# Kernel optimization log

Measured on AMD Instinct MI355X. Metric: run time of the kernel, lower is better.

The kernel has to match this reference:

```python
import jax, jax.numpy as jnp
import numpy as np

B, D, N, OUT, H = 32768, 256, 4, 512, 4
DH = D // H


def _layer_norm(x, g, b, eps=1e-5):
    mu = jnp.mean(x, axis=-1, keepdims=True)
    var = jnp.mean(jnp.square(x - mu), axis=-1, keepdims=True)
    return (x - mu) * jax.lax.rsqrt(var + eps) * g + b


def setup_inputs() -> dict:
    key = jax.random.key(0)
    ks = jax.random.split(key, 32)
    s = lambda i, shape, scale=0.02: (jax.random.normal(ks[i], shape, jnp.float32) * scale)
    inp = {
        'w0': jax.random.normal(ks[0], (B, D), jnp.float32),
        'w1': jax.random.normal(ks[1], (B, D), jnp.float32),
        'w2': jax.random.normal(ks[2], (B, D), jnp.float32),
        'w3': jax.random.normal(ks[3], (B, D), jnp.float32),
        'regime': jax.random.uniform(ks[4], (B, 4), jnp.float32),
        'tf_weights': jnp.array([0.5, 1.0, 1.5, 2.0], jnp.float32),
        'in_proj_w': s(5, (3 * D, D)),
        'in_proj_b': s(6, (3 * D,)),
        'out_proj_w': s(7, (D, D)),
        'out_proj_b': s(8, (D,)),
        'ln1_g': jnp.ones((D,), jnp.float32),
        'ln1_b': jnp.zeros((D,), jnp.float32),
        'sg_w': s(9, (D, 4)),
        'sg_b': s(10, (D,)),
        'sb_w': s(11, (D, 4)),
        'sb_b': s(12, (D,)),
        'f1_w': s(13, (2 * OUT, D * N)),
        'f1_b': s(14, (2 * OUT,)),
        'f2_w': s(15, (OUT, 2 * OUT)),
        'f2_b': s(16, (OUT,)),
        'ln2_g': jnp.ones((OUT,), jnp.float32),
        'ln2_b': jnp.zeros((OUT,), jnp.float32),
        'a1_w': s(17, (128, D * N)),
        'a1_b': s(18, (128,)),
        'a2_w': s(19, (1, 128)),
        'a2_b': s(20, (1,)),
    }
    return inp


def _forward(w0, w1, w2, w3, regime, tf_weights, in_proj_w, in_proj_b,
             out_proj_w, out_proj_b, ln1_g, ln1_b, sg_w, sg_b, sb_w, sb_b,
             f1_w, f1_b, f2_w, f2_b, ln2_g, ln2_b, a1_w, a1_b, a2_w, a2_b):
    weights = jax.nn.softmax(tf_weights)  # [N]
    wav = jnp.stack([w0, w1, w2, w3], axis=1)  # [B, N, D]
    weighted = wav * weights[None, :, None]    # [B, N, D]
    query = weighted[:, 0, :]                  # [B, D]

    # MultiheadAttention: q_len=1, kv_len=N, H heads
    wq, wk, wv = in_proj_w[:D], in_proj_w[D:2 * D], in_proj_w[2 * D:]
    bq, bk, bv = in_proj_b[:D], in_proj_b[D:2 * D], in_proj_b[2 * D:]
    q = (query @ wq.T + bq).reshape(B, H, DH)              # [B, H, Dh]
    k = (weighted @ wk.T + bk).reshape(B, N, H, DH)        # [B, N, H, Dh]
    v = (weighted @ wv.T + bv).reshape(B, N, H, DH)
    scores = jnp.einsum('bhd,bnhd->bhn', q, k) / jnp.sqrt(jnp.float32(DH))
    attn = jax.nn.softmax(scores, axis=-1)                 # [B, H, N]
    ctx = jnp.einsum('bhn,bnhd->bhd', attn, v).reshape(B, D)
    attn_out = ctx @ out_proj_w.T + out_proj_b             # [B, D]

    entry = _layer_norm(query + attn_out, ln1_g, ln1_b)    # [B, D]
    gamma = regime @ sg_w.T + sg_b
    beta = regime @ sb_w.T + sb_b
    entry = entry * (1.0 + gamma) + beta                   # FiLM

    cat = jnp.concatenate([entry, weighted[:, 1, :], weighted[:, 2, :], weighted[:, 3, :]], axis=-1)  # [B, D*N]
    h = jax.nn.gelu(cat @ f1_w.T + f1_b, approximate=False)
    fused = _layer_norm(h @ f2_w.T + f2_b, ln2_g, ln2_b)   # [B, OUT]

    a = jax.nn.gelu(cat @ a1_w.T + a1_b, approximate=False)
    alignment = jax.nn.sigmoid(a @ a2_w.T + a2_b)          # [B, 1]
    return fused, alignment


def reference(w0, w1, w2, w3, regime, tf_weights, in_proj_w, in_proj_b,
              out_proj_w, out_proj_b, ln1_g, ln1_b, sg_w, sg_b, sb_w, sb_b,
              f1_w, f1_b, f2_w, f2_b, ln2_g, ln2_b, a1_w, a1_b, a2_w, a2_b):
    return _forward(w0, w1, w2, w3, regime, tf_weights, in_proj_w, in_proj_b,
                    out_proj_w, out_proj_b, ln1_g, ln1_b, sg_w, sg_b, sb_w, sb_b,
                    f1_w, f1_b, f2_w, f2_b, ln2_g, ln2_b, a1_w, a1_b, a2_w, a2_b)
```

## Files before the change

kernel.cpp:

```cpp
#include <hip/hip_runtime.h>
#include <math.h>

#define NB 32768

typedef unsigned short u16;
typedef __attribute__((ext_vector_type(4))) float f32x4;
typedef __attribute__((ext_vector_type(8))) short bf16x8;

__device__ __forceinline__ float bf2f(u16 u){ return __uint_as_float(((unsigned int)u)<<16); }
__device__ __forceinline__ u16 f2bf(float f){
    unsigned int x = __float_as_uint(f);
    x += 0x7fffu + ((x>>16)&1u);
    return (u16)(x>>16);
}
__device__ __forceinline__ float gelu_f(float x){
    float z = fabsf(x) * 0.70710678118654752f;
    float t = __builtin_amdgcn_rcpf(1.0f + 0.3275911f*z);
    float p = t*(0.254829592f + t*(-0.284496736f + t*(1.421413741f + t*(-1.453152027f + t*1.061405429f))));
    float e = __expf(-z*z);
    float erf_abs = 1.0f - p*e;
    float erfv = copysignf(erf_abs, x);
    return 0.5f*x*(1.0f + erfv);
}

__device__ __forceinline__ void gload16(const void* g, void* l){
    __builtin_amdgcn_global_load_lds(
        (const __attribute__((address_space(1))) unsigned int*)g,
        (__attribute__((address_space(3))) unsigned int*)l, 16, 0, 0);
}

__global__ __launch_bounds__(256) void prep_kernel(
    const float* __restrict__ w0, const float* __restrict__ w1,
    const float* __restrict__ w2, const float* __restrict__ w3,
    const float* __restrict__ tfw, u16* __restrict__ wcat)
{
    float t0=tfw[0], t1=tfw[1], t2=tfw[2], t3=tfw[3];
    float m = fmaxf(fmaxf(t0,t1), fmaxf(t2,t3));
    float e0=expf(t0-m), e1=expf(t1-m), e2=expf(t2-m), e3=expf(t3-m);
    float inv = 1.0f/(e0+e1+e2+e3);
    float s0=e0*inv, s1=e1*inv, s2=e2*inv, s3=e3*inv;

    int idx = blockIdx.x*256 + threadIdx.x;
    int b  = idx >> 6;
    int d4 = (idx & 63) << 2;
    size_t src = (size_t)b*256 + d4;
    float4 a0 = *reinterpret_cast<const float4*>(w0 + src);
    float4 a1 = *reinterpret_cast<const float4*>(w1 + src);
    float4 a2 = *reinterpret_cast<const float4*>(w2 + src);
    float4 a3 = *reinterpret_cast<const float4*>(w3 + src);
    size_t dst = (size_t)b*1024 + d4;
    ushort4 o;
    o.x=f2bf(a0.x*s0); o.y=f2bf(a0.y*s0); o.z=f2bf(a0.z*s0); o.w=f2bf(a0.w*s0);
    *reinterpret_cast<ushort4*>(wcat + dst) = o;
    o.x=f2bf(a1.x*s1); o.y=f2bf(a1.y*s1); o.z=f2bf(a1.z*s1); o.w=f2bf(a1.w*s1);
    *reinterpret_cast<ushort4*>(wcat + dst + 256) = o;
    o.x=f2bf(a2.x*s2); o.y=f2bf(a2.y*s2); o.z=f2bf(a2.z*s2); o.w=f2bf(a2.w*s2);
    *reinterpret_cast<ushort4*>(wcat + dst + 512) = o;
    o.x=f2bf(a3.x*s3); o.y=f2bf(a3.y*s3); o.z=f2bf(a3.z*s3); o.w=f2bf(a3.w*s3);
    *reinterpret_cast<ushort4*>(wcat + dst + 768) = o;
}

__global__ __launch_bounds__(256) void conv1_kernel(const float* __restrict__ s, u16* __restrict__ d){
    int i = blockIdx.x*256 + threadIdx.x;
    float4 v = reinterpret_cast<const float4*>(s)[i];
    ushort4 o; o.x=f2bf(v.x); o.y=f2bf(v.y); o.z=f2bf(v.z); o.w=f2bf(v.w);
    reinterpret_cast<ushort4*>(d)[i] = o;
}

__global__ __launch_bounds__(256) void conv2_kernel(
    const float* __restrict__ s0, u16* __restrict__ d0,
    const float* __restrict__ s1, u16* __restrict__ d1,
    const float* __restrict__ s2, u16* __restrict__ d2,
    const float* __restrict__ s3, u16* __restrict__ d3)
{
    int i = blockIdx.x*256 + threadIdx.x;
    const float* s; u16* d; int off;
    if      (i < 16384) { s=s0; d=d0; off=i; }
    else if (i < 278528){ s=s1; d=d1; off=i-16384; }
    else if (i < 409600){ s=s2; d=d2; off=i-278528; }
    else                { s=s3; d=d3; off=i-409600; }
    float4 v = reinterpret_cast<const float4*>(s)[off];
    ushort4 o; o.x=f2bf(v.x); o.y=f2bf(v.y); o.z=f2bf(v.z); o.w=f2bf(v.w);
    reinterpret_cast<ushort4*>(d)[off] = o;
}

template<int ACT>
__global__ __launch_bounds__(256) void mgemm_kernel(
    const u16* __restrict__ A, int lda,
    const u16* __restrict__ W, int ldw,
    const float* __restrict__ bias,
    u16* __restrict__ C, int ldc, int K)
{
    __shared__ __align__(16) u16 sA[4096];
    __shared__ __align__(16) u16 sB[4096];

    const int tid  = threadIdx.x;
    const int lane = tid & 63;
    const int wid  = tid >> 6;
    const int wr   = wid >> 1, wc = wid & 1;
    const int row0 = blockIdx.x << 7, col0 = blockIdx.y << 7;

    const int e0 = tid << 3,          r0s = e0 >> 5, c0s = e0 & 31;
    const int e1 = (256 + tid) << 3,  r1s = e1 >> 5, c1s = e1 & 31;
    const u16* gA0 = A + (size_t)(row0 + r0s)*lda + c0s;
    const u16* gA1 = A + (size_t)(row0 + r1s)*lda + c1s;
    const u16* gB0 = W + (size_t)(col0 + r0s)*ldw + c0s;
    const u16* gB1 = W + (size_t)(col0 + r1s)*ldw + c1s;
    u16* lA0 = sA + (wid << 9);
    u16* lA1 = sA + 2048 + (wid << 9);
    u16* lB0 = sB + (wid << 9);
    u16* lB1 = sB + 2048 + (wid << 9);

    const int la  = lane & 15;
    const int lk  = (lane >> 4) << 3;
    const int hi4 = (lane >> 4) << 2;
    const u16* rA = sA + (((wr << 6) + la) << 5) + lk;
    const u16* rB = sB + (((wc << 6) + la) << 5) + lk;

    f32x4 acc[4][4];
    {
        f32x4 binit[4];
        #pragma unroll
        for (int n=0;n<4;n++){
            float4 b4 = *reinterpret_cast<const float4*>(bias + col0 + (wc<<6) + (n<<4) + hi4);
            binit[n] = (f32x4){b4.x, b4.y, b4.z, b4.w};
        }
        #pragma unroll
        for (int m=0;m<4;m++)
            #pragma unroll
            for (int n=0;n<4;n++) acc[m][n] = binit[n];
    }

    for (int k0 = 0; k0 < K; k0 += 32){
        gload16(gA0 + k0, lA0);
        gload16(gA1 + k0, lA1);
        gload16(gB0 + k0, lB0);
        gload16(gB1 + k0, lB1);
        __syncthreads();
        bf16x8 af[4], bf[4];
        #pragma unroll
        for (int m=0;m<4;m++) af[m] = *reinterpret_cast<const bf16x8*>(rA + (m << 9));
        #pragma unroll
        for (int n=0;n<4;n++) bf[n] = *reinterpret_cast<const bf16x8*>(rB + (n << 9));
        #pragma unroll
        for (int m=0;m<4;m++)
            #pragma unroll
            for (int n=0;n<4;n++)
                acc[m][n] = __builtin_amdgcn_mfma_f32_16x16x32_bf16(bf[n], af[m], acc[m][n], 0, 0, 0);
        __syncthreads();
    }

    #pragma unroll
    for (int m=0;m<4;m++){
        const int grow = row0 + (wr << 6) + (m << 4) + la;
        u16* crow = C + (size_t)grow*ldc + col0 + (wc << 6) + hi4;
        #pragma unroll
        for (int n=0;n<4;n++){
            f32x4 v = acc[m][n];
            float x0=v[0], x1=v[1], x2=v[2], x3=v[3];
            if (ACT == 1){ x0=gelu_f(x0); x1=gelu_f(x1); x2=gelu_f(x2); x3=gelu_f(x3); }
            ushort4 o; o.x=f2bf(x0); o.y=f2bf(x1); o.z=f2bf(x2); o.w=f2bf(x3);
            *reinterpret_cast<ushort4*>(crow + (n << 4)) = o;
        }
    }
}

template<int ACT>
__global__ __launch_bounds__(512) void gemm256p_kernel(
    const u16* __restrict__ A, int lda,
    const u16* __restrict__ W, int ldw,
    const float* __restrict__ bias,
    u16* __restrict__ C, int ldc, int K)
{
    __shared__ __align__(16) u16 sT[65536];

    const int tid  = threadIdx.x;
    const int lane = tid & 63;
    const int wid  = tid >> 6;
    const int wr   = wid >> 2;
    const int wc   = wid & 3;
    const int row0 = blockIdx.x << 8, col0 = blockIdx.y << 8;

    const int la = lane & 15;
    const int hi = lane >> 4;

    f32x4 acc[8][4];
    {
        f32x4 binit[4];
        #pragma unroll
        for (int n=0;n<4;n++){
            float4 b4 = *reinterpret_cast<const float4*>(bias + col0 + (wc<<6) + (n<<4) + (hi<<2));
            binit[n] = (f32x4){b4.x, b4.y, b4.z, b4.w};
        }
        #pragma unroll
        for (int m=0;m<8;m++)
            #pragma unroll
            for (int n=0;n<4;n++) acc[m][n] = binit[n];
    }

    const int rs = (wid << 4) + (lane >> 3);
    const int cs = ((lane & 7) ^ ((lane >> 3) & 7)) << 3;
    const u16* gA0 = A + (size_t)(row0 + rs)*lda + cs;
    const u16* gA1 = gA0 + (size_t)128*lda;
    const u16* gB0 = W + (size_t)(col0 + rs)*ldw + cs;
    const u16* gB1 = gB0 + (size_t)128*ldw;
    const int ldsw = (wid << 4) * 64;

    const int cph0 = (hi ^ (la & 7)) << 3;
    const u16* rAbase = sT + ((wr << 7) + la)*64;
    const u16* rBbase = sT + 16384 + ((wc << 6) + la)*64;

    const int NT = K >> 6;

    gload16(gB0, sT + 16384 + ldsw);          gload16(gB0 + 8*(size_t)ldw, sT + 16384 + ldsw + 512);
    gload16(gB1, sT + 16384 + 8192 + ldsw);   gload16(gB1 + 8*(size_t)ldw, sT + 16384 + 8192 + ldsw + 512);
    gload16(gA0, sT + ldsw);                  gload16(gA0 + 8*(size_t)lda, sT + ldsw + 512);
    gload16(gA1, sT + 8192 + ldsw);           gload16(gA1 + 8*(size_t)lda, sT + 8192 + ldsw + 512);

    for (int t = 0; t < NT; ++t){
        const int b  = (t & 1) << 15;
        const int bn = b ^ 32768;
        const int stg = (t + 1 < NT);
        const int kb = (t + 1) << 6;

#define STAGE_HALF(GP, LD, DOFF) \
        { gload16(GP + kb, sT + bn + (DOFF) + ldsw); \
          gload16(GP + kb + 8*(size_t)(LD), sT + bn + (DOFF) + ldsw + 512); }

#define PHASE(P) { \
        if ((P)==0){ \
            if (stg) { STAGE_HALF(gB0, ldw, 16384) } \
            if (stg) { asm volatile("s_waitcnt vmcnt(2)" ::: "memory"); } \
            else     { asm volatile("s_waitcnt vmcnt(0)" ::: "memory"); } \
        } \
        if ((P)==1 && stg) { STAGE_HALF(gB1, ldw, 16384 + 8192) } \
        if ((P)==2 && stg) { STAGE_HALF(gA0, lda, 0) } \
        if ((P)==3 && stg) { STAGE_HALF(gA1, lda, 8192) } \
        asm volatile("" ::: "memory"); \
        __builtin_amdgcn_s_barrier(); \
        __builtin_amdgcn_sched_barrier(0); \
        asm volatile("" ::: "memory"); \
        { \
            const int co = cph0 ^ (((P)>>1) << 5); \
            const u16* rA = rAbase + b + (((P)&1) << 12) + co; \
            const u16* rB = rBbase + b + co; \
            bf16x8 af0 = *reinterpret_cast<const bf16x8*>(rA); \
            bf16x8 af1 = *reinterpret_cast<const bf16x8*>(rA + 1024); \
            bf16x8 af2 = *reinterpret_cast<const bf16x8*>(rA + 2048); \
            bf16x8 af3 = *reinterpret_cast<const bf16x8*>(rA + 3072); \
            bf16x8 bf0 = *reinterpret_cast<const bf16x8*>(rB); \
            bf16x8 bf1 = *reinterpret_cast<const bf16x8*>(rB + 1024); \
            bf16x8 bf2 = *reinterpret_cast<const bf16x8*>(rB + 2048); \
            bf16x8 bf3 = *reinterpret_cast<const bf16x8*>(rB + 3072); \
            const int mb = ((P)&1) << 2; \
            __builtin_amdgcn_s_setprio(1); \
            acc[mb+0][0] = __builtin_amdgcn_mfma_f32_16x16x32_bf16(bf0, af0, acc[mb+0][0], 0,0,0); \
            acc[mb+0][1] = __builtin_amdgcn_mfma_f32_16x16x32_bf16(bf1, af0, acc[mb+0][1], 0,0,0); \
            acc[mb+0][2] = __builtin_amdgcn_mfma_f32_16x16x32_bf16(bf2, af0, acc[mb+0][2], 0,0,0); \
            acc[mb+0][3] = __builtin_amdgcn_mfma_f32_16x16x32_bf16(bf3, af0, acc[mb+0][3], 0,0,0); \
            acc[mb+1][0] = __builtin_amdgcn_mfma_f32_16x16x32_bf16(bf0, af1, acc[mb+1][0], 0,0,0); \
            acc[mb+1][1] = __builtin_amdgcn_mfma_f32_16x16x32_bf16(bf1, af1, acc[mb+1][1], 0,0,0); \
            acc[mb+1][2] = __builtin_amdgcn_mfma_f32_16x16x32_bf16(bf2, af1, acc[mb+1][2], 0,0,0); \
            acc[mb+1][3] = __builtin_amdgcn_mfma_f32_16x16x32_bf16(bf3, af1, acc[mb+1][3], 0,0,0); \
            acc[mb+2][0] = __builtin_amdgcn_mfma_f32_16x16x32_bf16(bf0, af2, acc[mb+2][0], 0,0,0); \
            acc[mb+2][1] = __builtin_amdgcn_mfma_f32_16x16x32_bf16(bf1, af2, acc[mb+2][1], 0,0,0); \
            acc[mb+2][2] = __builtin_amdgcn_mfma_f32_16x16x32_bf16(bf2, af2, acc[mb+2][2], 0,0,0); \
            acc[mb+2][3] = __builtin_amdgcn_mfma_f32_16x16x32_bf16(bf3, af2, acc[mb+2][3], 0,0,0); \
            acc[mb+3][0] = __builtin_amdgcn_mfma_f32_16x16x32_bf16(bf0, af3, acc[mb+3][0], 0,0,0); \
            acc[mb+3][1] = __builtin_amdgcn_mfma_f32_16x16x32_bf16(bf1, af3, acc[mb+3][1], 0,0,0); \
            acc[mb+3][2] = __builtin_amdgcn_mfma_f32_16x16x32_bf16(bf2, af3, acc[mb+3][2], 0,0,0); \
            acc[mb+3][3] = __builtin_amdgcn_mfma_f32_16x16x32_bf16(bf3, af3, acc[mb+3][3], 0,0,0); \
            __builtin_amdgcn_s_setprio(0); \
        } \
        __builtin_amdgcn_sched_barrier(0); \
        asm volatile("" ::: "memory"); \
        __builtin_amdgcn_s_barrier(); }

        PHASE(0)
        PHASE(1)
        PHASE(2)
        PHASE(3)
#undef PHASE
#undef STAGE_HALF
    }

    #pragma unroll
    for (int m=0;m<8;m++){
        const int grow = row0 + (wr << 7) + (m << 4) + la;
        u16* crow = C + (size_t)grow*ldc + col0 + (wc << 6) + (hi << 2);
        #pragma unroll
        for (int n=0;n<4;n++){
            f32x4 v = acc[m][n];
            float x0=v[0], x1=v[1], x2=v[2], x3=v[3];
            if (ACT == 1){ x0=gelu_f(x0); x1=gelu_f(x1); x2=gelu_f(x2); x3=gelu_f(x3); }
            ushort4 o; o.x=f2bf(x0); o.y=f2bf(x1); o.z=f2bf(x2); o.w=f2bf(x3);
            *reinterpret_cast<ushort4*>(crow + (n << 4)) = o;
        }
    }
}

__global__ __launch_bounds__(256) void attn_kernel(
    const u16* __restrict__ q, const u16* __restrict__ kv,
    u16* __restrict__ ctx)
{
    __shared__ float sQ[256], sK[1024], sV[1024], sS[16], sA[16];
    const int b = blockIdx.x, t = threadIdx.x;
    sQ[t] = bf2f(q[(size_t)b*256 + t]);
    #pragma unroll
    for (int n=0;n<4;n++){
        sK[n*256+t] = bf2f(kv[(size_t)b*2048 + n*512 + t]);
        sV[n*256+t] = bf2f(kv[(size_t)b*2048 + n*512 + 256 + t]);
    }
    __syncthreads();
    if (t < 16){
        int h = t>>2, n = t&3;
        float s = 0.f;
        const int o = h*64;
        #pragma unroll
        for (int dh=0; dh<64; ++dh) s += sQ[o+dh]*sK[n*256+o+dh];
        sS[t] = s * 0.125f;
    }
    __syncthreads();
    if (t < 4){
        float a0=sS[t*4+0], a1=sS[t*4+1], a2=sS[t*4+2], a3=sS[t*4+3];
        float m = fmaxf(fmaxf(a0,a1), fmaxf(a2,a3));
        float e0=expf(a0-m), e1=expf(a1-m), e2=expf(a2-m), e3=expf(a3-m);
        float inv = 1.0f/(e0+e1+e2+e3);
        sA[t*4+0]=e0*inv; sA[t*4+1]=e1*inv; sA[t*4+2]=e2*inv; sA[t*4+3]=e3*inv;
    }
    __syncthreads();
    const int h = t>>6;
    float c = sA[h*4+0]*sV[t] + sA[h*4+1]*sV[256+t] + sA[h*4+2]*sV[512+t] + sA[h*4+3]*sV[768+t];
    ctx[(size_t)b*256 + t] = f2bf(c);
}

__global__ __launch_bounds__(256) void lnfilm_kernel(
    u16* __restrict__ wcat, const u16* __restrict__ ao, const float* __restrict__ regime,
    const float* __restrict__ sgw, const float* __restrict__ sgb,
    const float* __restrict__ sbw, const float* __restrict__ sbb,
    const float* __restrict__ g1, const float* __restrict__ b1)
{
    const int b = blockIdx.x, t = threadIdx.x;
    float x = bf2f(wcat[(size_t)b*1024 + t]) + bf2f(ao[(size_t)b*256 + t]);
    float s = x, q = x*x;
    #pragma unroll
    for (int o=32;o;o>>=1){ s += __shfl_xor(s,o); q += __shfl_xor(q,o); }
    __shared__ float rs[4], rq[4];
    if ((t&63)==0){ rs[t>>6]=s; rq[t>>6]=q; }
    __syncthreads();
    s = rs[0]+rs[1]+rs[2]+rs[3];
    q = rq[0]+rq[1]+rq[2]+rq[3];
    float mu  = s*(1.0f/256.0f);
    float var = q*(1.0f/256.0f) - mu*mu;
    float rstd = rsqrtf(var + 1e-5f);
    float r0=regime[b*4+0], r1=regime[b*4+1], r2=regime[b*4+2], r3=regime[b*4+3];
    float gam = r0*sgw[t*4+0]+r1*sgw[t*4+1]+r2*sgw[t*4+2]+r3*sgw[t*4+3]+sgb[t];
    float bet = r0*sbw[t*4+0]+r1*sbw[t*4+1]+r2*sbw[t*4+2]+r3*sbw[t*4+3]+sbb[t];
    float e = ((x-mu)*rstd*g1[t]+b1[t])*(1.0f+gam)+bet;
    wcat[(size_t)b*1024 + t] = f2bf(e);
}

__global__ __launch_bounds__(256) void ln2_kernel(
    const u16* __restrict__ t1, const float* __restrict__ g, const float* __restrict__ bt,
    float* __restrict__ out)
{
    const int b = blockIdx.x, t = threadIdx.x;
    float x0 = bf2f(t1[(size_t)b*512 + t]);
    float x1 = bf2f(t1[(size_t)b*512 + 256 + t]);
    float s = x0+x1, q = x0*x0 + x1*x1;
    #pragma unroll
    for (int o=32;o;o>>=1){ s += __shfl_xor(s,o); q += __shfl_xor(q,o); }
    __shared__ float rs[4], rq[4];
    if ((t&63)==0){ rs[t>>6]=s; rq[t>>6]=q; }
    __syncthreads();
    s = rs[0]+rs[1]+rs[2]+rs[3];
    q = rq[0]+rq[1]+rq[2]+rq[3];
    float mu  = s*(1.0f/512.0f);
    float var = q*(1.0f/512.0f) - mu*mu;
    float rstd = rsqrtf(var + 1e-5f);
    out[(size_t)b*512 + t]       = (x0-mu)*rstd*g[t]     + bt[t];
    out[(size_t)b*512 + 256 + t] = (x1-mu)*rstd*g[256+t] + bt[256+t];
}

__global__ __launch_bounds__(64) void a2_kernel(
    const u16* __restrict__ a, const float* __restrict__ a2w, const float* __restrict__ a2b,
    float* __restrict__ out)
{
    const int b = blockIdx.x, t = threadIdx.x;
    float s = bf2f(a[(size_t)b*128 + t])*a2w[t] + bf2f(a[(size_t)b*128 + 64 + t])*a2w[64+t];
    #pragma unroll
    for (int o=32;o;o>>=1) s += __shfl_xor(s,o);
    if (t==0) out[b] = 1.0f/(1.0f+expf(-(s + a2b[0])));
}

extern "C" void kernel_launch(void* const* d_in, const int* in_sizes, int n_in,
                              void* d_out, int out_size, void* d_ws, size_t ws_size,
                              hipStream_t stream) {
    const float* w0   = (const float*)d_in[0];
    const float* w1   = (const float*)d_in[1];
    const float* w2   = (const float*)d_in[2];
    const float* w3   = (const float*)d_in[3];
    const float* regime = (const float*)d_in[4];
    const float* tfw  = (const float*)d_in[5];
    const float* in_proj_w = (const float*)d_in[6];
    const float* in_proj_b = (const float*)d_in[7];
    const float* out_proj_w = (const float*)d_in[8];
    const float* out_proj_b = (const float*)d_in[9];
    const float* ln1_g = (const float*)d_in[10];
    const float* ln1_b = (const float*)d_in[11];
    const float* sg_w = (const float*)d_in[12];
    const float* sg_b = (const float*)d_in[13];
    const float* sb_w = (const float*)d_in[14];
    const float* sb_b = (const float*)d_in[15];
    const float* f1_w = (const float*)d_in[16];
    const float* f1_b = (const float*)d_in[17];
    const float* f2_w = (const float*)d_in[18];
    const float* f2_b = (const float*)d_in[19];
    const float* ln2_g = (const float*)d_in[20];
    const float* ln2_b = (const float*)d_in[21];
    const float* a1_w = (const float*)d_in[22];
    const float* a1_b = (const float*)d_in[23];
    const float* a2_w = (const float*)d_in[24];
    const float* a2_b = (const float*)d_in[25];

    char* ws = (char*)d_ws;
    u16* wcat  = (u16*)(ws);
    u16* qbuf  = (u16*)(ws + 67108864ull);
    u16* kvbuf = (u16*)(ws + 83886080ull);
    u16* aobuf = (u16*)(ws + 218103808ull);
    u16* hbuf  = kvbuf;
    u16* t1buf = (u16*)(ws + 150994944ull);
    u16* abuf  = aobuf;
    u16* ipw   = aobuf;
    u16* wbf   = (u16*)(ws + 184549376ull);
    u16* opw   = wbf;
    u16* f1w   = wbf + 65536;
    u16* f2w   = wbf + 1114112;
    u16* a1w   = wbf + 1638400;

    float* out_fused = (float*)d_out;
    float* out_align = (float*)d_out + (size_t)NB*512;

    prep_kernel<<<NB*64/256, 256, 0, stream>>>(w0,w1,w2,w3,tfw,wcat);
    conv1_kernel<<<192, 256, 0, stream>>>(in_proj_w, ipw);
    mgemm_kernel<0><<<dim3(256, 2), 256, 0, stream>>>(wcat, 1024, ipw, 256, in_proj_b, qbuf, 256, 256);
    gemm256p_kernel<0><<<dim3(512, 2), 512, 0, stream>>>(wcat, 256, ipw+65536, 256, in_proj_b+256, kvbuf, 512, 256);
    attn_kernel<<<NB, 256, 0, stream>>>(qbuf, kvbuf, qbuf);
    conv2_kernel<<<1728, 256, 0, stream>>>(out_proj_w, opw, f1_w, f1w, f2_w, f2w, a1_w, a1w);
    mgemm_kernel<0><<<dim3(256, 2), 256, 0, stream>>>(qbuf, 256, opw, 256, out_proj_b, aobuf, 256, 256);
    lnfilm_kernel<<<NB, 256, 0, stream>>>(wcat, aobuf, regime, sg_w, sg_b, sb_w, sb_b, ln1_g, ln1_b);
    gemm256p_kernel<1><<<dim3(128, 4), 512, 0, stream>>>(wcat, 1024, f1w, 1024, f1_b, hbuf, 1024, 1024);
    gemm256p_kernel<0><<<dim3(128, 2), 512, 0, stream>>>(hbuf, 1024, f2w, 1024, f2_b, t1buf, 512, 1024);
    ln2_kernel<<<NB, 256, 0, stream>>>(t1buf, ln2_g, ln2_b, out_fused);
    mgemm_kernel<1><<<dim3(256, 1), 256, 0, stream>>>(wcat, 1024, a1w, 1024, a1_b, abuf, 128, 1024);
    a2_kernel<<<NB, 64, 0, stream>>>(abuf, a2_w, a2_b, out_align);
}
```

Measured before the change: 376.6 us.

## Merge prep/weight conversions, fuse a2 head into a1 GEMM, restructure gemm256p pipeline

```diff
diff --git a/kernel.cpp b/kernel.cpp
--- a/kernel.cpp
+++ b/kernel.cpp
@@ -29,59 +29,54 @@
         (__attribute__((address_space(3))) unsigned int*)l, 16, 0, 0);
 }
 
-__global__ __launch_bounds__(256) void prep_kernel(
+__global__ __launch_bounds__(256) void prepconv_kernel(
     const float* __restrict__ w0, const float* __restrict__ w1,
     const float* __restrict__ w2, const float* __restrict__ w3,
-    const float* __restrict__ tfw, u16* __restrict__ wcat)
-{
-    float t0=tfw[0], t1=tfw[1], t2=tfw[2], t3=tfw[3];
-    float m = fmaxf(fmaxf(t0,t1), fmaxf(t2,t3));
-    float e0=expf(t0-m), e1=expf(t1-m), e2=expf(t2-m), e3=expf(t3-m);
-    float inv = 1.0f/(e0+e1+e2+e3);
-    float s0=e0*inv, s1=e1*inv, s2=e2*inv, s3=e3*inv;
-
-    int idx = blockIdx.x*256 + threadIdx.x;
-    int b  = idx >> 6;
-    int d4 = (idx & 63) << 2;
-    size_t src = (size_t)b*256 + d4;
-    float4 a0 = *reinterpret_cast<const float4*>(w0 + src);
-    float4 a1 = *reinterpret_cast<const float4*>(w1 + src);
-    float4 a2 = *reinterpret_cast<const float4*>(w2 + src);
-    float4 a3 = *reinterpret_cast<const float4*>(w3 + src);
-    size_t dst = (size_t)b*1024 + d4;
-    ushort4 o;
-    o.x=f2bf(a0.x*s0); o.y=f2bf(a0.y*s0); o.z=f2bf(a0.z*s0); o.w=f2bf(a0.w*s0);
-    *reinterpret_cast<ushort4*>(wcat + dst) = o;
-    o.x=f2bf(a1.x*s1); o.y=f2bf(a1.y*s1); o.z=f2bf(a1.z*s1); o.w=f2bf(a1.w*s1);
-    *reinterpret_cast<ushort4*>(wcat + dst + 256) = o;
-    o.x=f2bf(a2.x*s2); o.y=f2bf(a2.y*s2); o.z=f2bf(a2.z*s2); o.w=f2bf(a2.w*s2);
-    *reinterpret_cast<ushort4*>(wcat + dst + 512) = o;
-    o.x=f2bf(a3.x*s3); o.y=f2bf(a3.y*s3); o.z=f2bf(a3.z*s3); o.w=f2bf(a3.w*s3);
-    *reinterpret_cast<ushort4*>(wcat + dst + 768) = o;
-}
-
-__global__ __launch_bounds__(256) void conv1_kernel(const float* __restrict__ s, u16* __restrict__ d){
-    int i = blockIdx.x*256 + threadIdx.x;
-    float4 v = reinterpret_cast<const float4*>(s)[i];
-    ushort4 o; o.x=f2bf(v.x); o.y=f2bf(v.y); o.z=f2bf(v.z); o.w=f2bf(v.w);
-    reinterpret_cast<ushort4*>(d)[i] = o;
-}
-
-__global__ __launch_bounds__(256) void conv2_kernel(
-    const float* __restrict__ s0, u16* __restrict__ d0,
-    const float* __restrict__ s1, u16* __restrict__ d1,
-    const float* __restrict__ s2, u16* __restrict__ d2,
-    const float* __restrict__ s3, u16* __restrict__ d3)
-{
-    int i = blockIdx.x*256 + threadIdx.x;
-    const float* s; u16* d; int off;
-    if      (i < 16384) { s=s0; d=d0; off=i; }
-    else if (i < 278528){ s=s1; d=d1; off=i-16384; }
-    else if (i < 409600){ s=s2; d=d2; off=i-278528; }
-    else                { s=s3; d=d3; off=i-409600; }
-    float4 v = reinterpret_cast<const float4*>(s)[off];
-    ushort4 o; o.x=f2bf(v.x); o.y=f2bf(v.y); o.z=f2bf(v.z); o.w=f2bf(v.w);
-    reinterpret_cast<ushort4*>(d)[off] = o;
+    const float* __restrict__ tfw, u16* __restrict__ wcat,
+    const float* __restrict__ ipw_s, u16* __restrict__ ipw_d,
+    const float* __restrict__ op_s,  u16* __restrict__ op_d,
+    const float* __restrict__ f1_s,  u16* __restrict__ f1_d,
+    const float* __restrict__ f2_s,  u16* __restrict__ f2_d,
+    const float* __restrict__ a1_s,  u16* __restrict__ a1_d)
+{
+    const int blk = blockIdx.x, tid = threadIdx.x;
+    if (blk < 8192){
+        float t0=tfw[0], t1=tfw[1], t2=tfw[2], t3=tfw[3];
+        float m = fmaxf(fmaxf(t0,t1), fmaxf(t2,t3));
+        float e0=expf(t0-m), e1=expf(t1-m), e2=expf(t2-m), e3=expf(t3-m);
+        float inv = 1.0f/(e0+e1+e2+e3);
+        float s0=e0*inv, s1=e1*inv, s2=e2*inv, s3=e3*inv;
+
+        int idx = blk*256 + tid;
+        int b  = idx >> 6;
+        int d4 = (idx & 63) << 2;
+        size_t src = (size_t)b*256 + d4;
+        float4 a0 = *reinterpret_cast<const float4*>(w0 + src);
+        float4 a1 = *reinterpret_cast<const float4*>(w1 + src);
+        float4 a2 = *reinterpret_cast<const float4*>(w2 + src);
+        float4 a3 = *reinterpret_cast<const float4*>(w3 + src);
+        size_t dst = (size_t)b*1024 + d4;
+        ushort4 o;
+        o.x=f2bf(a0.x*s0); o.y=f2bf(a0.y*s0); o.z=f2bf(a0.z*s0); o.w=f2bf(a0.w*s0);
+        *reinterpret_cast<ushort4*>(wcat + dst) = o;
+        o.x=f2bf(a1.x*s1); o.y=f2bf(a1.y*s1); o.z=f2bf(a1.z*s1); o.w=f2bf(a1.w*s1);
+        *reinterpret_cast<ushort4*>(wcat + dst + 256) = o;
+        o.x=f2bf(a2.x*s2); o.y=f2bf(a2.y*s2); o.z=f2bf(a2.z*s2); o.w=f2bf(a2.w*s2);
+        *reinterpret_cast<ushort4*>(wcat + dst + 512) = o;
+        o.x=f2bf(a3.x*s3); o.y=f2bf(a3.y*s3); o.z=f2bf(a3.z*s3); o.w=f2bf(a3.w*s3);
+        *reinterpret_cast<ushort4*>(wcat + dst + 768) = o;
+    } else {
+        int i = (blk - 8192)*256 + tid;
+        const float* s; u16* d; int off;
+        if      (i < 49152)  { s=ipw_s; d=ipw_d; off=i; }
+        else if (i < 65536)  { s=op_s;  d=op_d;  off=i-49152; }
+        else if (i < 327680) { s=f1_s;  d=f1_d;  off=i-65536; }
+        else if (i < 458752) { s=f2_s;  d=f2_d;  off=i-327680; }
+        else                 { s=a1_s;  d=a1_d;  off=i-458752; }
+        float4 v = reinterpret_cast<const float4*>(s)[off];
+        ushort4 o; o.x=f2bf(v.x); o.y=f2bf(v.y); o.z=f2bf(v.z); o.w=f2bf(v.w);
+        reinterpret_cast<ushort4*>(d)[off] = o;
+    }
 }
 
 template<int ACT>
@@ -89,7 +84,8 @@
     const u16* __restrict__ A, int lda,
     const u16* __restrict__ W, int ldw,
     const float* __restrict__ bias,
-    u16* __restrict__ C, int ldc, int K)
+    u16* __restrict__ C, int ldc, int K,
+    const float* __restrict__ a2w, const float* __restrict__ a2b, float* __restrict__ aln)
 {
     __shared__ __align__(16) u16 sA[4096];
     __shared__ __align__(16) u16 sB[4096];
@@ -150,6 +146,35 @@
         __syncthreads();
     }
 
+    if (ACT == 2){
+        float w4[4][4];
+        #pragma unroll
+        for (int n=0;n<4;n++){
+            float4 t4 = *reinterpret_cast<const float4*>(a2w + (wc<<6) + (n<<4) + hi4);
+            w4[n][0]=t4.x; w4[n][1]=t4.y; w4[n][2]=t4.z; w4[n][3]=t4.w;
+        }
+        float* red = reinterpret_cast<float*>(sA);
+        #pragma unroll
+        for (int m=0;m<4;m++){
+            float p = 0.f;
+            #pragma unroll
+            for (int n=0;n<4;n++){
+                f32x4 v = acc[m][n];
+                p += gelu_f(v[0])*w4[n][0] + gelu_f(v[1])*w4[n][1]
+                   + gelu_f(v[2])*w4[n][2] + gelu_f(v[3])*w4[n][3];
+            }
+            red[(((wr<<6) + (m<<4) + la) << 3) + (wc<<2) + (lane>>4)] = p;
+        }
+        __syncthreads();
+        if (tid < 128){
+            float s = 0.f;
+            #pragma unroll
+            for (int k2=0;k2<8;k2++) s += red[(tid<<3)+k2];
+            aln[row0 + tid] = 1.0f/(1.0f + __expf(-(s + a2b[0])));
+        }
+        return;
+    }
+
     #pragma unroll
     for (int m=0;m<4;m++){
         const int grow = row0 + (wr << 6) + (m << 4) + la;
@@ -213,76 +238,72 @@
     const int NT = K >> 6;
 
     gload16(gB0, sT + 16384 + ldsw);          gload16(gB0 + 8*(size_t)ldw, sT + 16384 + ldsw + 512);
-    gload16(gB1, sT + 16384 + 8192 + ldsw);   gload16(gB1 + 8*(size_t)ldw, sT + 16384 + 8192 + ldsw + 512);
+    gload16(gB1, sT + 24576 + ldsw);          gload16(gB1 + 8*(size_t)ldw, sT + 24576 + ldsw + 512);
     gload16(gA0, sT + ldsw);                  gload16(gA0 + 8*(size_t)lda, sT + ldsw + 512);
     gload16(gA1, sT + 8192 + ldsw);           gload16(gA1 + 8*(size_t)lda, sT + 8192 + ldsw + 512);
+
+#define STG(GP, LD, DOFF) \
+        gload16(GP + kb, sT + bn + (DOFF) + ldsw); \
+        gload16(GP + kb + 8*(size_t)(LD), sT + bn + (DOFF) + ldsw + 512);
+
+#define DSR(MH, KS) { \
+        const int co_ = cph0 ^ ((KS) << 5); \
+        const u16* rA_ = rAbase + b + ((MH) << 12) + co_; \
+        const u16* rB_ = rBbase + b + co_; \
+        af[0] = *reinterpret_cast<const bf16x8*>(rA_); \
+        af[1] = *reinterpret_cast<const bf16x8*>(rA_ + 1024); \
+        af[2] = *reinterpret_cast<const bf16x8*>(rA_ + 2048); \
+        af[3] = *reinterpret_cast<const bf16x8*>(rA_ + 3072); \
+        bf[0] = *reinterpret_cast<const bf16x8*>(rB_); \
+        bf[1] = *reinterpret_cast<const bf16x8*>(rB_ + 1024); \
+        bf[2] = *reinterpret_cast<const bf16x8*>(rB_ + 2048); \
+        bf[3] = *reinterpret_cast<const bf16x8*>(rB_ + 3072); }
+
+#define MFMA16(MB) { \
+        __builtin_amdgcn_s_setprio(1); \
+        _Pragma("unroll") \
+        for (int m=0;m<4;m++){ \
+            _Pragma("unroll") \
+            for (int n=0;n<4;n++) \
+                acc[(MB)+m][n] = __builtin_amdgcn_mfma_f32_16x16x32_bf16(bf[n], af[m], acc[(MB)+m][n], 0,0,0); \
+        } \
+        __builtin_amdgcn_s_setprio(0); }
 
     for (int t = 0; t < NT; ++t){
         const int b  = (t & 1) << 15;
         const int bn = b ^ 32768;
-        const int stg = (t + 1 < NT);
+        const bool stg = (t + 1 < NT);
         const int kb = (t + 1) << 6;
-
-#define STAGE_HALF(GP, LD, DOFF) \
-        { gload16(GP + kb, sT + bn + (DOFF) + ldsw); \
-          gload16(GP + kb + 8*(size_t)(LD), sT + bn + (DOFF) + ldsw + 512); }
-
-#define PHASE(P) { \
-        if ((P)==0){ \
-            if (stg) { STAGE_HALF(gB0, ldw, 16384) } \
-            if (stg) { asm volatile("s_waitcnt vmcnt(2)" ::: "memory"); } \
-            else     { asm volatile("s_waitcnt vmcnt(0)" ::: "memory"); } \
-        } \
-        if ((P)==1 && stg) { STAGE_HALF(gB1, ldw, 16384 + 8192) } \
-        if ((P)==2 && stg) { STAGE_HALF(gA0, lda, 0) } \
-        if ((P)==3 && stg) { STAGE_HALF(gA1, lda, 8192) } \
-        asm volatile("" ::: "memory"); \
-        __builtin_amdgcn_s_barrier(); \
-        __builtin_amdgcn_sched_barrier(0); \
-        asm volatile("" ::: "memory"); \
-        { \
-            const int co = cph0 ^ (((P)>>1) << 5); \
-            const u16* rA = rAbase + b + (((P)&1) << 12) + co; \
-            const u16* rB = rBbase + b + co; \
-            bf16x8 af0 = *reinterpret_cast<const bf16x8*>(rA); \
-            bf16x8 af1 = *reinterpret_cast<const bf16x8*>(rA + 1024); \
-            bf16x8 af2 = *reinterpret_cast<const bf16x8*>(rA + 2048); \
-            bf16x8 af3 = *reinterpret_cast<const bf16x8*>(rA + 3072); \
-            bf16x8 bf0 = *reinterpret_cast<const bf16x8*>(rB); \
-            bf16x8 bf1 = *reinterpret_cast<const bf16x8*>(rB + 1024); \
-            bf16x8 bf2 = *reinterpret_cast<const bf16x8*>(rB + 2048); \
-            bf16x8 bf3 = *reinterpret_cast<const bf16x8*>(rB + 3072); \
-            const int mb = ((P)&1) << 2; \
-            __builtin_amdgcn_s_setprio(1); \
-            acc[mb+0][0] = __builtin_amdgcn_mfma_f32_16x16x32_bf16(bf0, af0, acc[mb+0][0], 0,0,0); \
-            acc[mb+0][1] = __builtin_amdgcn_mfma_f32_16x16x32_bf16(bf1, af0, acc[mb+0][1], 0,0,0); \
-            acc[mb+0][2] = __builtin_amdgcn_mfma_f32_16x16x32_bf16(bf2, af0, acc[mb+0][2], 0,0,0); \
-            acc[mb+0][3] = __builtin_amdgcn_mfma_f32_16x16x32_bf16(bf3, af0, acc[mb+0][3], 0,0,0); \
-            acc[mb+1][0] = __builtin_amdgcn_mfma_f32_16x16x32_bf16(bf0, af1, acc[mb+1][0], 0,0,0); \
-            acc[mb+1][1] = __builtin_amdgcn_mfma_f32_16x16x32_bf16(bf1, af1, acc[mb+1][1], 0,0,0); \
-            acc[mb+1][2] = __builtin_amdgcn_mfma_f32_16x16x32_bf16(bf2, af1, acc[mb+1][2], 0,0,0); \
-            acc[mb+1][3] = __builtin_amdgcn_mfma_f32_16x16x32_bf16(bf3, af1, acc[mb+1][3], 0,0,0); \
-            acc[mb+2][0] = __builtin_amdgcn_mfma_f32_16x16x32_bf16(bf0, af2, acc[mb+2][0], 0,0,0); \
-            acc[mb+2][1] = __builtin_amdgcn_mfma_f32_16x16x32_bf16(bf1, af2, acc[mb+2][1], 0,0,0); \
-            acc[mb+2][2] = __builtin_amdgcn_mfma_f32_16x16x32_bf16(bf2, af2, acc[mb+2][2], 0,0,0); \
-            acc[mb+2][3] = __builtin_amdgcn_mfma_f32_16x16x32_bf16(bf3, af2, acc[mb+2][3], 0,0,0); \
-            acc[mb+3][0] = __builtin_amdgcn_mfma_f32_16x16x32_bf16(bf0, af3, acc[mb+3][0], 0,0,0); \
-            acc[mb+3][1] = __builtin_amdgcn_mfma_f32_16x16x32_bf16(bf1, af3, acc[mb+3][1], 0,0,0); \
-            acc[mb+3][2] = __builtin_amdgcn_mfma_f32_16x16x32_bf16(bf2, af3, acc[mb+3][2], 0,0,0); \
-            acc[mb+3][3] = __builtin_amdgcn_mfma_f32_16x16x32_bf16(bf3, af3, acc[mb+3][3], 0,0,0); \
-            __builtin_amdgcn_s_setprio(0); \
-        } \
-        __builtin_amdgcn_sched_barrier(0); \
-        asm volatile("" ::: "memory"); \
-        __builtin_amdgcn_s_barrier(); }
-
-        PHASE(0)
-        PHASE(1)
-        PHASE(2)
-        PHASE(3)
-#undef PHASE
-#undef STAGE_HALF
-    }
+        bf16x8 af[4], bf[4];
+
+        asm volatile("s_waitcnt vmcnt(0)" ::: "memory");
+        __builtin_amdgcn_s_barrier();
+        __builtin_amdgcn_sched_barrier(0);
+        DSR(0,0)
+        if (stg){ STG(gB0, ldw, 16384) }
+        MFMA16(0)
+        DSR(1,0)
+        if (stg){ STG(gB1, ldw, 24576) }
+        __builtin_amdgcn_sched_barrier(0);
+        __builtin_amdgcn_s_barrier();
+        __builtin_amdgcn_sched_barrier(0);
+        MFMA16(4)
+        DSR(0,1)
+        if (stg){ STG(gA0, lda, 0) }
+        __builtin_amdgcn_sched_barrier(0);
+        __builtin_amdgcn_s_barrier();
+        __builtin_amdgcn_sched_barrier(0);
+        MFMA16(0)
+        DSR(1,1)
+        if (stg){ STG(gA1, lda, 8192) }
+        __builtin_amdgcn_sched_barrier(0);
+        __builtin_amdgcn_s_barrier();
+        __builtin_amdgcn_sched_barrier(0);
+        MFMA16(4)
+    }
+#undef STG
+#undef DSR
+#undef MFMA16
 
     #pragma unroll
     for (int m=0;m<8;m++){
@@ -380,17 +401,6 @@
     float rstd = rsqrtf(var + 1e-5f);
     out[(size_t)b*512 + t]       = (x0-mu)*rstd*g[t]     + bt[t];
     out[(size_t)b*512 + 256 + t] = (x1-mu)*rstd*g[256+t] + bt[256+t];
-}
-
-__global__ __launch_bounds__(64) void a2_kernel(
-    const u16* __restrict__ a, const float* __restrict__ a2w, const float* __restrict__ a2b,
-    float* __restrict__ out)
-{
-    const int b = blockIdx.x, t = threadIdx.x;
-    float s = bf2f(a[(size_t)b*128 + t])*a2w[t] + bf2f(a[(size_t)b*128 + 64 + t])*a2w[64+t];
-    #pragma unroll
-    for (int o=32;o;o>>=1) s += __shfl_xor(s,o);
-    if (t==0) out[b] = 1.0f/(1.0f+expf(-(s + a2b[0])));
 }
 
 extern "C" void kernel_launch(void* const* d_in, const int* in_sizes, int n_in,
@@ -427,31 +437,28 @@
     u16* wcat  = (u16*)(ws);
     u16* qbuf  = (u16*)(ws + 67108864ull);
     u16* kvbuf = (u16*)(ws + 83886080ull);
-    u16* aobuf = (u16*)(ws + 218103808ull);
     u16* hbuf  = kvbuf;
     u16* t1buf = (u16*)(ws + 150994944ull);
-    u16* abuf  = aobuf;
-    u16* ipw   = aobuf;
-    u16* wbf   = (u16*)(ws + 184549376ull);
-    u16* opw   = wbf;
-    u16* f1w   = wbf + 65536;
-    u16* f2w   = wbf + 1114112;
-    u16* a1w   = wbf + 1638400;
+    u16* aobuf = (u16*)(ws + 184549376ull);
+    u16* wb    = (u16*)(ws + 218103808ull);
+    u16* ipw = wb;
+    u16* opw = wb + 196608;
+    u16* f1w = wb + 262144;
+    u16* f2w = wb + 1310720;
+    u16* a1w = wb + 1835008;
 
     float* out_fused = (float*)d_out;
     float* out_align = (float*)d_out + (size_t)NB*512;
 
-    prep_kernel<<<NB*64/256, 256, 0, stream>>>(w0,w1,w2,w3,tfw,wcat);
-    conv1_kernel<<<192, 256, 0, stream>>>(in_proj_w, ipw);
-    mgemm_kernel<0><<<dim3(256, 2), 256, 0, stream>>>(wcat, 1024, ipw, 256, in_proj_b, qbuf, 256, 256);
+    prepconv_kernel<<<10112, 256, 0, stream>>>(w0,w1,w2,w3,tfw,wcat,
+        in_proj_w,ipw, out_proj_w,opw, f1_w,f1w, f2_w,f2w, a1_w,a1w);
+    mgemm_kernel<0><<<dim3(256, 2), 256, 0, stream>>>(wcat, 1024, ipw, 256, in_proj_b, qbuf, 256, 256, nullptr, nullptr, nullptr);
     gemm256p_kernel<0><<<dim3(512, 2), 512, 0, stream>>>(wcat, 256, ipw+65536, 256, in_proj_b+256, kvbuf, 512, 256);
     attn_kernel<<<NB, 256, 0, stream>>>(qbuf, kvbuf, qbuf);
-    conv2_kernel<<<1728, 256, 0, stream>>>(out_proj_w, opw, f1_w, f1w, f2_w, f2w, a1_w, a1w);
-    mgemm_kernel<0><<<dim3(256, 2), 256, 0, stream>>>(qbuf, 256, opw, 256, out_proj_b, aobuf, 256, 256);
+    mgemm_kernel<0><<<dim3(256, 2), 256, 0, stream>>>(qbuf, 256, opw, 256, out_proj_b, aobuf, 256, 256, nullptr, nullptr, nullptr);
     lnfilm_kernel<<<NB, 256, 0, stream>>>(wcat, aobuf, regime, sg_w, sg_b, sb_w, sb_b, ln1_g, ln1_b);
     gemm256p_kernel<1><<<dim3(128, 4), 512, 0, stream>>>(wcat, 1024, f1w, 1024, f1_b, hbuf, 1024, 1024);
     gemm256p_kernel<0><<<dim3(128, 2), 512, 0, stream>>>(hbuf, 1024, f2w, 1024, f2_b, t1buf, 512, 1024);
     ln2_kernel<<<NB, 256, 0, stream>>>(t1buf, ln2_g, ln2_b, out_fused);
-    mgemm_kernel<1><<<dim3(256, 1), 256, 0, stream>>>(wcat, 1024, a1w, 1024, a1_b, abuf, 128, 1024);
-    a2_kernel<<<NB, 64, 0, stream>>>(abuf, a2_w, a2_b, out_align);
-}
+    mgemm_kernel<2><<<dim3(256, 1), 256, 0, stream>>>(wcat, 1024, a1w, 1024, a1_b, qbuf, 128, 1024, a2_w, a2_b, out_align);
+}
```

New measurement: 357.0 us. 5.2% less time.
